# Kernel optimization log

Hardware: AMD Instinct MI355X
Metric: run time of the kernel (lower is better)

Reference implementation:

```python
import jax, jax.numpy as jnp
import numpy as np

# simulation params from inputs_cell = (dt, (gamma, omega, n, eta, kappa, b), trainable_params)
DT = 1e-3
GAMMA = 0.3
NBAR = 2.0
ETA = 0.8
KAPPA = 0.9
B, T = 512, 4096


def setup_inputs() -> dict:
    key = jax.random.key(0)
    k1, = jax.random.split(key, 1)
    # measurement increments dy ~ sqrt(dt)-scaled noise, shape [B, T, 2]
    dy = jax.random.normal(k1, (B, T, 2), dtype=jnp.float32) * jnp.float32(np.sqrt(DT))
    # state = (<q>, <p>, Var[q], Var[p], Cov(q,p), t); start at vacuum-ish cov 0.5
    state0 = jnp.concatenate(
        [
            jnp.zeros((B, 2), jnp.float32),            # x
            0.5 * jnp.ones((B, 1), jnp.float32),       # vx
            0.5 * jnp.ones((B, 1), jnp.float32),       # vp
            jnp.zeros((B, 1), jnp.float32),            # cxp
            jnp.zeros((B, 1), jnp.float32),            # t
        ],
        axis=1,
    )
    omega_p = jnp.ones((1,), dtype=jnp.float32)  # trainable_params = 1.0
    return {"dy": dy, "state0": state0, "omega_p": omega_p}


def reference(dy, state0, omega_p):
    C = jnp.float32(np.sqrt(4.0 * ETA * KAPPA)) * jnp.array([[1.0, 0.0], [0.0, 0.0]], jnp.float32)
    D = jnp.float32(GAMMA * (NBAR + 0.5) + KAPPA) * jnp.eye(2, dtype=jnp.float32)
    J = jnp.array([[0.0, 1.0], [-1.0, 0.0]], jnp.float32)
    A = -0.5 * GAMMA * jnp.eye(2, dtype=jnp.float32) + omega_p[0] * J  # [2,2]

    dy_t_major = jnp.swapaxes(dy, 0, 1)  # [T, B, 2]

    def step(state, dy_t):
        x = state[:, :2]                                   # [B,2]
        vx, vp, cxp = state[:, 2], state[:, 3], state[:, 4]
        t = state[:, 5]
        cov = jnp.stack(
            [jnp.stack([vx, cxp], -1), jnp.stack([cxp, vp], -1)], -2
        )  # [B,2,2]
        xicov = jnp.einsum('bij,kj->bik', cov, C)          # cov @ C.T
        M = A - jnp.einsum('bij,jk->bik', xicov, C)        # A - xicov @ C
        dx = jnp.einsum('bij,bj->bi', M, x) * DT + jnp.einsum('bij,bj->bi', xicov, dy_t)
        dcov = DT * (
            jnp.einsum('bij,kj->bik', cov, A)              # cov @ A.T
            + jnp.einsum('ij,bjk->bik', A, cov)            # A @ cov
            + D
            - jnp.einsum('bij,bkj->bik', xicov, xicov)     # xicov @ xicov.T
        )
        ncov = cov + dcov
        nstate = jnp.concatenate(
            [x + dx, ncov[:, 0, 0:1], ncov[:, 1, 1:2], ncov[:, 1, 0:1], (t + DT)[:, None]],
            axis=1,
        )
        dy_hat = jnp.einsum('ij,bj->bi', C, x) * DT
        return nstate, dy_hat

    final_state, dy_hat = jax.lax.scan(step, state0, dy_t_major)
    return final_state, jnp.swapaxes(dy_hat, 0, 1)  # [B,6], [B,T,2]
```

## Files before the change

### kernel.cpp

```cpp
#include <hip/hip_runtime.h>
#include <math.h>


constexpr int T = 4096;
constexpr int B = 512;
constexpr int CH = 16;
constexpr int NC = T / CH;
constexpr int NSWEEP = 3;
constexpr int SB = 258;

constexpr int WS_T = 0;
constexpr int WS_H = 16384;
constexpr int WS_P = 24576;
constexpr int WS_F = 25600;

__global__ __launch_bounds__(256) void grnn_phaseA(
    const float* __restrict__ state0,
    const float* __restrict__ omega_p,
    float* __restrict__ ws)
{
    __shared__ float2 scovT[T];
    __shared__ float4 sS[NC];
    __shared__ float wtot[4][12];
    const int c  = threadIdx.x;
    const int l  = c & 63;
    const int wv = c >> 6;

    const float DT = 0.001f;
    const float w  = omega_p[0];
    const float k1 = 1.0f + DT * (-0.3f);
    const float k2 = DT * 2.0f * w;
    const float k3 = DT * 1.65f;
    const float k4 = DT * 2.88f;
    const float kw = DT * w;
    const float kA = 1.0f + DT * (-0.15f);
    const float cc = 1.69705627484771f;
    const float nk4 = -k4, n2k4 = -2.0f * k4;
    const float w2c = 2.0f * w;

    float vx = state0[2], vp = state0[3], cx = state0[4];
    float S0 = vx, S1 = vp, S2 = cx;
    {
        const int Q = c >> 2, r = c & 3;
        const float dt64 = 64.0f * DT;
        for (int i = 0; i < 64; ++i) {
            if (i == Q) { S0 = vx; S1 = vp; S2 = cx; }
            const float fvx = fmaf(-2.88f, vx * vx, fmaf(-0.3f, vx, fmaf(w2c, cx, 1.65f)));
            const float fvp = fmaf(-2.88f, cx * cx, fmaf(-0.3f, vp, fmaf(-w2c, cx, 1.65f)));
            const float fcx = fmaf(-2.88f, vx * cx, fmaf(-0.3f, cx, w * (vp - vx)));
            vx = fmaf(dt64, fvx, vx);
            vp = fmaf(dt64, fvp, vp);
            cx = fmaf(dt64, fcx, cx);
        }
        vx = S0; vp = S1; cx = S2;
        const float dt16 = 16.0f * DT;
        #pragma unroll
        for (int i = 0; i < 3; ++i) {
            if (i < r) {
                const float fvx = fmaf(-2.88f, vx * vx, fmaf(-0.3f, vx, fmaf(w2c, cx, 1.65f)));
                const float fvp = fmaf(-2.88f, cx * cx, fmaf(-0.3f, vp, fmaf(-w2c, cx, 1.65f)));
                const float fcx = fmaf(-2.88f, vx * cx, fmaf(-0.3f, cx, w * (vp - vx)));
                vx = fmaf(dt16, fvx, vx);
                vp = fmaf(dt16, fvp, vp);
                cx = fmaf(dt16, fcx, cx);
            }
        }
        S0 = vx; S1 = vp; S2 = cx;
    }
    sS[c] = make_float4(S0, S1, S2, 0.f);
    __syncthreads();

    for (int sw = 0; sw < NSWEEP; ++sw) {
        float vx0 = S0, vp0 = S1, cx0 = S2;
        float m00=1.f,m01=0.f,m02=0.f, m10=0.f,m11=1.f,m12=0.f, m20=0.f,m21=0.f,m22=1.f;
        #pragma unroll 4
        for (int j = 0; j < CH; ++j) {
            const float J00 = fmaf(n2k4, vx0, k1);
            const float J12 = fmaf(n2k4, cx0, -k2);
            const float J20 = fmaf(nk4, cx0, -kw);
            const float J22 = fmaf(nk4, vx0, k1);
            const float a00 = fmaf(J00, m00, k2 * m20);
            const float a01 = fmaf(J00, m01, k2 * m21);
            const float a02 = fmaf(J00, m02, k2 * m22);
            const float a10 = fmaf(k1, m10, J12 * m20);
            const float a11 = fmaf(k1, m11, J12 * m21);
            const float a12 = fmaf(k1, m12, J12 * m22);
            const float a20 = fmaf(J20, m00, fmaf(kw, m10, J22 * m20));
            const float a21 = fmaf(J20, m01, fmaf(kw, m11, J22 * m21));
            const float a22 = fmaf(J20, m02, fmaf(kw, m12, J22 * m22));
            m00 = a00; m01 = a01; m02 = a02;
            m10 = a10; m11 = a11; m12 = a12;
            m20 = a20; m21 = a21; m22 = a22;
            const float t1   = fmaf(nk4, vx0, k1);
            const float s1   = fmaf(k2, cx0, k3);
            const float mvx  = -kw * vx0;
            const float mm   = fmaf(kw, vp0, mvx);
            const float cxp2 = cx0 * cx0;
            const float uu   = fmaf(-k2, cx0, k3);
            const float in2  = fmaf(nk4, cxp2, uu);
            const float nvp  = fmaf(k1, vp0, in2);
            const float nvx  = fmaf(t1, vx0, s1);
            const float ncx  = fmaf(t1, cx0, mm);
            vx0 = nvx; cx0 = ncx; vp0 = nvp;
        }
        const float4 Sn = sS[(c + 1) & (NC - 1)];
        float d0 = vx0 - Sn.x, d1 = vp0 - Sn.y, d2 = cx0 - Sn.z;
        if (c == NC - 1) { d0 = 0.f; d1 = 0.f; d2 = 0.f; }
        for (int k = 1; k < 64; k <<= 1) {
            const float o00 = __shfl_up(m00, k), o01 = __shfl_up(m01, k), o02 = __shfl_up(m02, k);
            const float o10 = __shfl_up(m10, k), o11 = __shfl_up(m11, k), o12 = __shfl_up(m12, k);
            const float o20 = __shfl_up(m20, k), o21 = __shfl_up(m21, k), o22 = __shfl_up(m22, k);
            const float e0  = __shfl_up(d0, k),  e1  = __shfl_up(d1, k),  e2  = __shfl_up(d2, k);
            if (l >= k) {
                const float b00 = fmaf(m00, o00, fmaf(m01, o10, m02 * o20));
                const float b01 = fmaf(m00, o01, fmaf(m01, o11, m02 * o21));
                const float b02 = fmaf(m00, o02, fmaf(m01, o12, m02 * o22));
                const float b10 = fmaf(m10, o00, fmaf(m11, o10, m12 * o20));
                const float b11 = fmaf(m10, o01, fmaf(m11, o11, m12 * o21));
                const float b12 = fmaf(m10, o02, fmaf(m11, o12, m12 * o22));
                const float b20 = fmaf(m20, o00, fmaf(m21, o10, m22 * o20));
                const float b21 = fmaf(m20, o01, fmaf(m21, o11, m22 * o21));
                const float b22 = fmaf(m20, o02, fmaf(m21, o12, m22 * o22));
                const float nd0 = fmaf(m00, e0, fmaf(m01, e1, fmaf(m02, e2, d0)));
                const float nd1 = fmaf(m10, e0, fmaf(m11, e1, fmaf(m12, e2, d1)));
                const float nd2 = fmaf(m20, e0, fmaf(m21, e1, fmaf(m22, e2, d2)));
                m00 = b00; m01 = b01; m02 = b02;
                m10 = b10; m11 = b11; m12 = b12;
                m20 = b20; m21 = b21; m22 = b22;
                d0 = nd0; d1 = nd1; d2 = nd2;
            }
        }
        if (l == 63) {
            float* wt = wtot[wv];
            wt[0]=m00; wt[1]=m01; wt[2]=m02; wt[3]=m10; wt[4]=m11; wt[5]=m12;
            wt[6]=m20; wt[7]=m21; wt[8]=m22; wt[9]=d0; wt[10]=d1; wt[11]=d2;
        }
        __syncthreads();
        float pq0 = 0.f, pq1 = 0.f, pq2 = 0.f;
        for (int w2 = 0; w2 < wv; ++w2) {
            const float* wt = wtot[w2];
            const float n0 = fmaf(wt[0],pq0,fmaf(wt[1],pq1,fmaf(wt[2],pq2,wt[9])));
            const float n1 = fmaf(wt[3],pq0,fmaf(wt[4],pq1,fmaf(wt[5],pq2,wt[10])));
            const float n2 = fmaf(wt[6],pq0,fmaf(wt[7],pq1,fmaf(wt[8],pq2,wt[11])));
            pq0 = n0; pq1 = n1; pq2 = n2;
        }
        const float qf0 = fmaf(m00,pq0,fmaf(m01,pq1,fmaf(m02,pq2,d0)));
        const float qf1 = fmaf(m10,pq0,fmaf(m11,pq1,fmaf(m12,pq2,d1)));
        const float qf2 = fmaf(m20,pq0,fmaf(m21,pq1,fmaf(m22,pq2,d2)));
        float E0 = __shfl_up(qf0, 1), E1 = __shfl_up(qf1, 1), E2 = __shfl_up(qf2, 1);
        if (l == 0) { E0 = pq0; E1 = pq1; E2 = pq2; }
        S0 += E0; S1 += E1; S2 += E2;
        __syncthreads();
        sS[c] = make_float4(S0, S1, S2, 0.f);
        __syncthreads();
    }

    float vx0 = S0, vp0 = S1, cx0 = S2;
    #pragma unroll 4
    for (int j = 0; j < CH; ++j) {
        scovT[j * NC + c] = make_float2(vx0, cx0);
        const float t1   = fmaf(nk4, vx0, k1);
        const float s1   = fmaf(k2, cx0, k3);
        const float mvx  = -kw * vx0;
        const float mm   = fmaf(kw, vp0, mvx);
        const float cxp2 = cx0 * cx0;
        const float uu   = fmaf(-k2, cx0, k3);
        const float in2  = fmaf(nk4, cxp2, uu);
        const float nvp  = fmaf(k1, vp0, in2);
        const float nvx  = fmaf(t1, vx0, s1);
        const float ncx  = fmaf(t1, cx0, mm);
        vx0 = nvx; cx0 = ncx; vp0 = nvp;
    }
    if (c == NC - 1) {
        ws[WS_F]     = vx0;
        ws[WS_F + 1] = vp0;
        ws[WS_F + 2] = cx0;
        ws[WS_F + 3] = state0[5] + 4096.0f * 0.001f;
    }

    float r00 = 1.f, r01 = 0.f, r10 = 0.f, r11 = 1.f;
    float4* TtabT = (float4*)(ws + WS_T);
    float2* HtabT = (float2*)(ws + WS_H);
    #pragma unroll 4
    for (int j = CH - 1; j >= 0; --j) {
        const float2 vc = scovT[j * NC + c];
        const float T00 = fmaf(nk4, vc.x, kA);
        const float T10 = fmaf(nk4, vc.y, -kw);
        const float g0  = cc * vc.x;
        const float g1  = cc * vc.y;
        HtabT[j * NC + c] = make_float2(fmaf(r00, g0, r01 * g1), fmaf(r10, g0, r11 * g1));
        TtabT[j * NC + c] = make_float4(T00, T10, g0, g1);
        const float n00 = fmaf(r00, T00, r01 * T10);
        const float n01 = fmaf(r00, kw,  r01 * kA);
        const float n10 = fmaf(r10, T00, r11 * T10);
        const float n11 = fmaf(r10, kw,  r11 * kA);
        r00 = n00; r01 = n01; r10 = n10; r11 = n11;
    }
    ((float4*)(ws + WS_P))[c] = make_float4(r00, r01, r10, r11);
}

__global__ __launch_bounds__(256) void grnn_phaseBCD(
    const float* __restrict__ dy,
    const float* __restrict__ state0,
    const float* __restrict__ omega_p,
    float* __restrict__ out,
    const float* __restrict__ ws)
{
    __shared__ float sbuf[CH * SB];
    __shared__ float wtot[4][6];
    const int b  = blockIdx.x;
    const int c  = threadIdx.x;
    const int l  = c & 63;
    const int wv = c >> 6;

    const float DT = 0.001f;
    const float w  = omega_p[0];
    const float kw = DT * w;
    const float kA = 1.0f + DT * (-0.15f);
    const float cc = 1.69705627484771f;
    const float kcDT = cc * DT;

    const float4* TtabT = (const float4*)(ws + WS_T);
    const float2* HtabT = (const float2*)(ws + WS_H);

    const float* dyb = dy + (size_t)b * (T * 2);
    #pragma unroll
    for (int k = 0; k < 8; ++k) {
        const float4 d = *(const float4*)(dyb + 4 * (k * 256 + c));
        const int t0 = 2 * (k * 256 + c);
        const int j0 = t0 & 15;
        const int c0 = t0 >> 4;
        sbuf[j0 * SB + c0]       = d.x;
        sbuf[(j0 + 1) * SB + c0] = d.z;
    }
    __syncthreads();

    float q0 = 0.f, q1 = 0.f;
    #pragma unroll 4
    for (int j = 0; j < CH; ++j) {
        const float d0 = sbuf[j * SB + c];
        const float2 h = HtabT[j * NC + c];
        q0 = fmaf(h.x, d0, q0);
        q1 = fmaf(h.y, d0, q1);
    }
    const float4 Pv = ((const float4*)(ws + WS_P))[c];
    float p00 = Pv.x, p01 = Pv.y, p10 = Pv.z, p11 = Pv.w;

    for (int d = 1; d < 64; d <<= 1) {
        const float o00 = __shfl_up(p00, d), o01 = __shfl_up(p01, d);
        const float o10 = __shfl_up(p10, d), o11 = __shfl_up(p11, d);
        const float oq0 = __shfl_up(q0, d),  oq1 = __shfl_up(q1, d);
        if (l >= d) {
            const float n00 = fmaf(p00, o00, p01 * o10);
            const float n01 = fmaf(p00, o01, p01 * o11);
            const float n10 = fmaf(p10, o00, p11 * o10);
            const float n11 = fmaf(p10, o01, p11 * o11);
            const float nq0 = fmaf(p00, oq0, fmaf(p01, oq1, q0));
            const float nq1 = fmaf(p10, oq0, fmaf(p11, oq1, q1));
            p00 = n00; p01 = n01; p10 = n10; p11 = n11;
            q0 = nq0; q1 = nq1;
        }
    }
    if (l == 63) {
        float* wt = wtot[wv];
        wt[0] = p00; wt[1] = p01; wt[2] = p10; wt[3] = p11; wt[4] = q0; wt[5] = q1;
    }
    __syncthreads();
    float f00 = 1.f, f01 = 0.f, f10 = 0.f, f11 = 1.f, fq0 = 0.f, fq1 = 0.f;
    for (int w2 = 0; w2 < wv; ++w2) {
        const float* wt = wtot[w2];
        const float t00 = wt[0], t01 = wt[1], t10 = wt[2], t11 = wt[3];
        const float tq0 = wt[4], tq1 = wt[5];
        const float n00 = fmaf(t00, f00, t01 * f10);
        const float n01 = fmaf(t00, f01, t01 * f11);
        const float n10 = fmaf(t10, f00, t11 * f10);
        const float n11 = fmaf(t10, f01, t11 * f11);
        const float nq0 = fmaf(t00, fq0, fmaf(t01, fq1, tq0));
        const float nq1 = fmaf(t10, fq0, fmaf(t11, fq1, tq1));
        f00 = n00; f01 = n01; f10 = n10; f11 = n11; fq0 = nq0; fq1 = nq1;
    }
    const float F00 = fmaf(p00, f00, p01 * f10);
    const float F01 = fmaf(p00, f01, p01 * f11);
    const float F10 = fmaf(p10, f00, p11 * f10);
    const float F11 = fmaf(p10, f01, p11 * f11);
    const float Fq0 = fmaf(p00, fq0, fmaf(p01, fq1, q0));
    const float Fq1 = fmaf(p10, fq0, fmaf(p11, fq1, q1));
    float e00 = __shfl_up(F00, 1), e01 = __shfl_up(F01, 1);
    float e10 = __shfl_up(F10, 1), e11 = __shfl_up(F11, 1);
    float eq0 = __shfl_up(Fq0, 1), eq1 = __shfl_up(Fq1, 1);
    if (l == 0) { e00 = f00; e01 = f01; e10 = f10; e11 = f11; eq0 = fq0; eq1 = fq1; }

    const float xi0 = state0[b * 6 + 0];
    const float xi1 = state0[b * 6 + 1];
    float x0 = fmaf(e00, xi0, fmaf(e01, xi1, eq0));
    float x1 = fmaf(e10, xi0, fmaf(e11, xi1, eq1));

    #pragma unroll 4
    for (int j = 0; j < CH; ++j) {
        const float d0 = sbuf[j * SB + c];
        const float4 Tt = TtabT[j * NC + c];
        const float h0  = kcDT * x0;
        const float nx0 = fmaf(Tt.x, x0, fmaf(kw, x1, Tt.z * d0));
        const float nx1 = fmaf(Tt.y, x0, fmaf(kA, x1, Tt.w * d0));
        sbuf[j * SB + c] = h0;
        x0 = nx0; x1 = nx1;
    }

    if (c == NC - 1) {
        float* os = out + b * 6;
        os[0] = x0;           os[1] = x1;
        os[2] = ws[WS_F];     os[3] = ws[WS_F + 1];
        os[4] = ws[WS_F + 2]; os[5] = ws[WS_F + 3];
    }
    __syncthreads();

    float* dyh = out + B * 6 + (size_t)b * (T * 2);
    #pragma unroll
    for (int k = 0; k < 8; ++k) {
        const int t0 = 2 * (k * 256 + c);
        const int j0 = t0 & 15;
        const int c0 = t0 >> 4;
        const float h0 = sbuf[j0 * SB + c0];
        const float h1 = sbuf[(j0 + 1) * SB + c0];
        *(float4*)(dyh + 4 * (k * 256 + c)) = make_float4(h0, 0.f, h1, 0.f);
    }
}

extern "C" void kernel_launch(void* const* d_in, const int* in_sizes, int n_in,
                              void* d_out, int out_size, void* d_ws, size_t ws_size,
                              hipStream_t stream) {
    const float* dy     = (const float*)d_in[0];
    const float* state0 = (const float*)d_in[1];
    const float* omega  = (const float*)d_in[2];
    float* out = (float*)d_out;
    float* ws  = (float*)d_ws;
    grnn_phaseA<<<1, 256, 0, stream>>>(state0, omega, ws);
    grnn_phaseBCD<<<B, 256, 0, stream>>>(dy, state0, omega, out, ws);
}
```

Measured before the change: 91.59 us.

## Fuse covariance precompute into per-batch kernel, recomputing tables in each block

Merges the single-block covariance/table kernel into the per-batch kernel so each block redundantly recomputes the batch-independent covariance trajectory and propagator in shared memory. This removes the second launch, the serial dependency between kernels, and global workspace writes and reads of the T/H/P tables. The dy load is issued before the covariance computation, so its latency can overlap that compute. In exchange every block repeats the sequential covariance scan and uses more shared memory, which may reduce occupancy.

Result: no change. 92.62 us (+1.1%).

```diff
diff --git a/kernel.cpp b/kernel.cpp
--- a/kernel.cpp
+++ b/kernel.cpp
@@ -9,19 +9,18 @@
 constexpr int NSWEEP = 3;
 constexpr int SB = 258;
 
-constexpr int WS_T = 0;
-constexpr int WS_H = 16384;
-constexpr int WS_P = 24576;
-constexpr int WS_F = 25600;
-
-__global__ __launch_bounds__(256) void grnn_phaseA(
+__global__ __launch_bounds__(256) void grnn_fused(
+    const float* __restrict__ dy,
     const float* __restrict__ state0,
     const float* __restrict__ omega_p,
-    float* __restrict__ ws)
+    float* __restrict__ out)
 {
     __shared__ float2 scovT[T];
+    __shared__ float sbuf[CH * SB];
     __shared__ float4 sS[NC];
-    __shared__ float wtot[4][12];
+    __shared__ float wtotA[4][12];
+    __shared__ float wtotX[4][6];
+    const int b  = blockIdx.x;
     const int c  = threadIdx.x;
     const int l  = c & 63;
     const int wv = c >> 6;
@@ -35,8 +34,20 @@
     const float kw = DT * w;
     const float kA = 1.0f + DT * (-0.15f);
     const float cc = 1.69705627484771f;
+    const float kcDT = cc * DT;
     const float nk4 = -k4, n2k4 = -2.0f * k4;
     const float w2c = 2.0f * w;
+
+    const float* dyb = dy + (size_t)b * (T * 2);
+    #pragma unroll
+    for (int k = 0; k < 8; ++k) {
+        const float4 d = *(const float4*)(dyb + 4 * (k * 256 + c));
+        const int t0 = 2 * (k * 256 + c);
+        const int j0 = t0 & 15;
+        const int c0 = t0 >> 4;
+        sbuf[j0 * SB + c0]       = d.x;
+        sbuf[(j0 + 1) * SB + c0] = d.z;
+    }
 
     float vx = state0[2], vp = state0[3], cx = state0[4];
     float S0 = vx, S1 = vp, S2 = cx;
@@ -131,14 +142,14 @@
             }
         }
         if (l == 63) {
-            float* wt = wtot[wv];
+            float* wt = wtotA[wv];
             wt[0]=m00; wt[1]=m01; wt[2]=m02; wt[3]=m10; wt[4]=m11; wt[5]=m12;
             wt[6]=m20; wt[7]=m21; wt[8]=m22; wt[9]=d0; wt[10]=d1; wt[11]=d2;
         }
         __syncthreads();
         float pq0 = 0.f, pq1 = 0.f, pq2 = 0.f;
         for (int w2 = 0; w2 < wv; ++w2) {
-            const float* wt = wtot[w2];
+            const float* wt = wtotA[w2];
             const float n0 = fmaf(wt[0],pq0,fmaf(wt[1],pq1,fmaf(wt[2],pq2,wt[9])));
             const float n1 = fmaf(wt[3],pq0,fmaf(wt[4],pq1,fmaf(wt[5],pq2,wt[10])));
             const float n2 = fmaf(wt[6],pq0,fmaf(wt[7],pq1,fmaf(wt[8],pq2,wt[11])));
@@ -155,96 +166,49 @@
         __syncthreads();
     }
 
-    float vx0 = S0, vp0 = S1, cx0 = S2;
-    #pragma unroll 4
-    for (int j = 0; j < CH; ++j) {
-        scovT[j * NC + c] = make_float2(vx0, cx0);
-        const float t1   = fmaf(nk4, vx0, k1);
-        const float s1   = fmaf(k2, cx0, k3);
-        const float mvx  = -kw * vx0;
-        const float mm   = fmaf(kw, vp0, mvx);
-        const float cxp2 = cx0 * cx0;
-        const float uu   = fmaf(-k2, cx0, k3);
-        const float in2  = fmaf(nk4, cxp2, uu);
-        const float nvp  = fmaf(k1, vp0, in2);
-        const float nvx  = fmaf(t1, vx0, s1);
-        const float ncx  = fmaf(t1, cx0, mm);
-        vx0 = nvx; cx0 = ncx; vp0 = nvp;
-    }
-    if (c == NC - 1) {
-        ws[WS_F]     = vx0;
-        ws[WS_F + 1] = vp0;
-        ws[WS_F + 2] = cx0;
-        ws[WS_F + 3] = state0[5] + 4096.0f * 0.001f;
-    }
+    float fvx = 0.f, fvp = 0.f, fcx = 0.f;
+    {
+        float vx0 = S0, vp0 = S1, cx0 = S2;
+        #pragma unroll 4
+        for (int j = 0; j < CH; ++j) {
+            scovT[j * NC + c] = make_float2(vx0, cx0);
+            const float t1   = fmaf(nk4, vx0, k1);
+            const float s1   = fmaf(k2, cx0, k3);
+            const float mvx  = -kw * vx0;
+            const float mm   = fmaf(kw, vp0, mvx);
+            const float cxp2 = cx0 * cx0;
+            const float uu   = fmaf(-k2, cx0, k3);
+            const float in2  = fmaf(nk4, cxp2, uu);
+            const float nvp  = fmaf(k1, vp0, in2);
+            const float nvx  = fmaf(t1, vx0, s1);
+            const float ncx  = fmaf(t1, cx0, mm);
+            vx0 = nvx; cx0 = ncx; vp0 = nvp;
+        }
+        fvx = vx0; fvp = vp0; fcx = cx0;
+    }
+    __syncthreads();
 
     float r00 = 1.f, r01 = 0.f, r10 = 0.f, r11 = 1.f;
-    float4* TtabT = (float4*)(ws + WS_T);
-    float2* HtabT = (float2*)(ws + WS_H);
+    float q0 = 0.f, q1 = 0.f;
     #pragma unroll 4
     for (int j = CH - 1; j >= 0; --j) {
         const float2 vc = scovT[j * NC + c];
+        const float d0v = sbuf[j * SB + c];
         const float T00 = fmaf(nk4, vc.x, kA);
         const float T10 = fmaf(nk4, vc.y, -kw);
         const float g0  = cc * vc.x;
         const float g1  = cc * vc.y;
-        HtabT[j * NC + c] = make_float2(fmaf(r00, g0, r01 * g1), fmaf(r10, g0, r11 * g1));
-        TtabT[j * NC + c] = make_float4(T00, T10, g0, g1);
+        const float h0  = fmaf(r00, g0, r01 * g1);
+        const float h1  = fmaf(r10, g0, r11 * g1);
+        q0 = fmaf(h0, d0v, q0);
+        q1 = fmaf(h1, d0v, q1);
         const float n00 = fmaf(r00, T00, r01 * T10);
         const float n01 = fmaf(r00, kw,  r01 * kA);
         const float n10 = fmaf(r10, T00, r11 * T10);
         const float n11 = fmaf(r10, kw,  r11 * kA);
         r00 = n00; r01 = n01; r10 = n10; r11 = n11;
     }
-    ((float4*)(ws + WS_P))[c] = make_float4(r00, r01, r10, r11);
-}
-
-__global__ __launch_bounds__(256) void grnn_phaseBCD(
-    const float* __restrict__ dy,
-    const float* __restrict__ state0,
-    const float* __restrict__ omega_p,
-    float* __restrict__ out,
-    const float* __restrict__ ws)
-{
-    __shared__ float sbuf[CH * SB];
-    __shared__ float wtot[4][6];
-    const int b  = blockIdx.x;
-    const int c  = threadIdx.x;
-    const int l  = c & 63;
-    const int wv = c >> 6;
-
-    const float DT = 0.001f;
-    const float w  = omega_p[0];
-    const float kw = DT * w;
-    const float kA = 1.0f + DT * (-0.15f);
-    const float cc = 1.69705627484771f;
-    const float kcDT = cc * DT;
-
-    const float4* TtabT = (const float4*)(ws + WS_T);
-    const float2* HtabT = (const float2*)(ws + WS_H);
-
-    const float* dyb = dy + (size_t)b * (T * 2);
-    #pragma unroll
-    for (int k = 0; k < 8; ++k) {
-        const float4 d = *(const float4*)(dyb + 4 * (k * 256 + c));
-        const int t0 = 2 * (k * 256 + c);
-        const int j0 = t0 & 15;
-        const int c0 = t0 >> 4;
-        sbuf[j0 * SB + c0]       = d.x;
-        sbuf[(j0 + 1) * SB + c0] = d.z;
-    }
-    __syncthreads();
-
-    float q0 = 0.f, q1 = 0.f;
-    #pragma unroll 4
-    for (int j = 0; j < CH; ++j) {
-        const float d0 = sbuf[j * SB + c];
-        const float2 h = HtabT[j * NC + c];
-        q0 = fmaf(h.x, d0, q0);
-        q1 = fmaf(h.y, d0, q1);
-    }
-    const float4 Pv = ((const float4*)(ws + WS_P))[c];
-    float p00 = Pv.x, p01 = Pv.y, p10 = Pv.z, p11 = Pv.w;
+    float p00 = r00, p01 = r01, p10 = r10, p11 = r11;
 
     for (int d = 1; d < 64; d <<= 1) {
         const float o00 = __shfl_up(p00, d), o01 = __shfl_up(p01, d);
@@ -262,13 +226,13 @@
         }
     }
     if (l == 63) {
-        float* wt = wtot[wv];
+        float* wt = wtotX[wv];
         wt[0] = p00; wt[1] = p01; wt[2] = p10; wt[3] = p11; wt[4] = q0; wt[5] = q1;
     }
     __syncthreads();
     float f00 = 1.f, f01 = 0.f, f10 = 0.f, f11 = 1.f, fq0 = 0.f, fq1 = 0.f;
     for (int w2 = 0; w2 < wv; ++w2) {
-        const float* wt = wtot[w2];
+        const float* wt = wtotX[w2];
         const float t00 = wt[0], t01 = wt[1], t10 = wt[2], t11 = wt[3];
         const float tq0 = wt[4], tq1 = wt[5];
         const float n00 = fmaf(t00, f00, t01 * f10);
@@ -297,20 +261,24 @@
 
     #pragma unroll 4
     for (int j = 0; j < CH; ++j) {
-        const float d0 = sbuf[j * SB + c];
-        const float4 Tt = TtabT[j * NC + c];
+        const float2 vc = scovT[j * NC + c];
+        const float d0v = sbuf[j * SB + c];
+        const float T00 = fmaf(nk4, vc.x, kA);
+        const float T10 = fmaf(nk4, vc.y, -kw);
+        const float g0  = cc * vc.x;
+        const float g1  = cc * vc.y;
         const float h0  = kcDT * x0;
-        const float nx0 = fmaf(Tt.x, x0, fmaf(kw, x1, Tt.z * d0));
-        const float nx1 = fmaf(Tt.y, x0, fmaf(kA, x1, Tt.w * d0));
+        const float nx0 = fmaf(T00, x0, fmaf(kw, x1, g0 * d0v));
+        const float nx1 = fmaf(T10, x0, fmaf(kA, x1, g1 * d0v));
         sbuf[j * SB + c] = h0;
         x0 = nx0; x1 = nx1;
     }
 
     if (c == NC - 1) {
         float* os = out + b * 6;
-        os[0] = x0;           os[1] = x1;
-        os[2] = ws[WS_F];     os[3] = ws[WS_F + 1];
-        os[4] = ws[WS_F + 2]; os[5] = ws[WS_F + 3];
+        os[0] = x0;  os[1] = x1;
+        os[2] = fvx; os[3] = fvp; os[4] = fcx;
+        os[5] = state0[5] + 4096.0f * 0.001f;
     }
     __syncthreads();
 
@@ -333,7 +301,5 @@
     const float* state0 = (const float*)d_in[1];
     const float* omega  = (const float*)d_in[2];
     float* out = (float*)d_out;
-    float* ws  = (float*)d_ws;
-    grnn_phaseA<<<1, 256, 0, stream>>>(state0, omega, ws);
-    grnn_phaseBCD<<<B, 256, 0, stream>>>(dy, state0, omega, out, ws);
+    grnn_fused<<<B, 256, 0, stream>>>(dy, state0, omega, out);
 }
```
